# Performance work log

Hardware: AMD Instinct MI355X
Metric: run time of the kernel (lower is better)

The kernel has to match this reference:

```python
import jax, jax.numpy as jnp
import numpy as np

N_NODES = 100000
N_EDGES = 3200000
F_IN = 256
HID = 64
N_CLS = 16


def setup_inputs() -> dict:
    key = jax.random.key(0)
    ks = jax.random.split(key, 12)
    x = jax.random.normal(ks[0], (N_NODES, F_IN), dtype=jnp.float32)
    edge_index = jax.random.randint(ks[1], (2, N_EDGES), 0, N_NODES, dtype=jnp.int32)
    w_mul = jax.random.normal(ks[2], (N_EDGES, 1), dtype=jnp.float32)
    s1 = 1.0 / np.sqrt(F_IN)
    s2 = 1.0 / np.sqrt(HID)
    # layer 1 params
    lin1_w = jax.random.uniform(ks[3], (HID, F_IN), minval=-s1, maxval=s1, dtype=jnp.float32)
    lin1_b = jax.random.uniform(ks[4], (HID,), minval=-s1, maxval=s1, dtype=jnp.float32)
    mlp1_w0 = jax.random.uniform(ks[5], (HID, 1), minval=-1.0, maxval=1.0, dtype=jnp.float32)
    mlp1_w1 = jax.random.uniform(ks[6], (HID, HID), minval=-s2, maxval=s2, dtype=jnp.float32)
    mlp1_b1 = jax.random.uniform(ks[7], (HID,), minval=-s2, maxval=s2, dtype=jnp.float32)
    # layer 2 params
    lin2_w = jax.random.uniform(ks[8], (N_CLS, HID), minval=-s2, maxval=s2, dtype=jnp.float32)
    lin2_b = jax.random.uniform(ks[9], (N_CLS,), minval=-s2, maxval=s2, dtype=jnp.float32)
    mlp2_w0 = jax.random.uniform(ks[10], (HID, 1), minval=-1.0, maxval=1.0, dtype=jnp.float32)
    mlp2_w1 = jax.random.uniform(ks[11], (N_CLS, HID), minval=-s2, maxval=s2, dtype=jnp.float32)
    mlp2_b1 = jnp.zeros((N_CLS,), dtype=jnp.float32)
    return dict(x=x, edge_index=edge_index, w_mul=w_mul,
                lin1_w=lin1_w, lin1_b=lin1_b, mlp1_w0=mlp1_w0, mlp1_w1=mlp1_w1, mlp1_b1=mlp1_b1,
                lin2_w=lin2_w, lin2_b=lin2_b, mlp2_w0=mlp2_w0, mlp2_w1=mlp2_w1, mlp2_b1=mlp2_b1)


def curv_layer(x, src, dst, w_mul, lin_w, lin_b, m_w0, m_w1, m_b1, n_nodes):
    # dense projection: [N, out]
    h = x @ lin_w.T + lin_b
    # per-edge weight MLP: Linear(1,HID,no bias) -> LeakyReLU(0.2) -> Linear(HID,out,bias)
    ew = jax.nn.leaky_relu(w_mul @ m_w0.T, negative_slope=0.2) @ m_w1.T + m_b1  # [E, out]
    # segment softmax keyed by source node (PyG softmax(out_weight, edge_index[0]))
    emax = jax.ops.segment_max(ew, src, num_segments=n_nodes)  # [N, out]
    e = jnp.exp(ew - emax[src])
    esum = jax.ops.segment_sum(e, src, num_segments=n_nodes)
    alpha = e / (esum[src] + 1e-16)  # [E, out]
    # message = alpha * x_j (x_j = h[src]); scatter-add at destination
    msg = alpha * h[src]
    return jax.ops.segment_sum(msg, dst, num_segments=n_nodes)  # [N, out]


def reference(x, edge_index, w_mul,
              lin1_w, lin1_b, mlp1_w0, mlp1_w1, mlp1_b1,
              lin2_w, lin2_b, mlp2_w0, mlp2_w1, mlp2_b1):
    src, dst = edge_index[0], edge_index[1]
    n = x.shape[0]
    # eval mode: dropout(p=0.8) is identity
    h = curv_layer(x, src, dst, w_mul, lin1_w, lin1_b, mlp1_w0, mlp1_w1, mlp1_b1, n)
    h = jax.nn.elu(h)
    h = curv_layer(h, src, dst, w_mul, lin2_w, lin2_b, mlp2_w0, mlp2_w1, mlp2_b1, n)
    return jax.nn.log_softmax(h, axis=1)
```

## Files before the change

kernel.cpp:

```cpp
#include <hip/hip_runtime.h>
#include <math.h>

#define FIN 256
#define HID 64
#define NCLS 16
#define BSH 8
#define BWD (1 << BSH)
#define NBKMAX 512
#define CAP 9216
#define CHUNK_S 8192
#define CHUNK_D 4096

typedef __attribute__((ext_vector_type(8))) short bf16x8;
typedef __attribute__((ext_vector_type(4))) float f32x4;

__global__ __launch_bounds__(512) void init_kernel(int* gcur_s, int* gcur_d) {
    int tid = threadIdx.x;
    gcur_s[tid] = tid * CAP;
    gcur_d[tid] = tid * CAP;
}

__global__ __launch_bounds__(512) void stage_kernel(const int* __restrict__ ei,
                                                    const float* __restrict__ w,
                                                    int* gcur_s, int* gcur_d,
                                                    unsigned int* st_s, uint2* st_d,
                                                    int E, int nchunk_s) {
    __shared__ int lh[NBKMAX];
    __shared__ int lofs[NBKMAX];
    __shared__ int lcur[NBKMAX];
    __shared__ int gbase[NBKMAX];
    __shared__ int wsum[8];
    __shared__ uint2 buf2[CHUNK_D];
    unsigned int* buf1 = (unsigned int*)buf2;
    int tid = threadIdx.x;
    int wv = tid >> 6, lane = tid & 63;
    int side = (blockIdx.x >= nchunk_s) ? 1 : 0;
    lh[tid] = 0;
    __syncthreads();
    if (!side) {
        int base = blockIdx.x * CHUNK_S;
        #pragma unroll
        for (int j = 0; j < CHUNK_S / 512; j++) {
            int e = base + tid + j * 512;
            if (e < E) atomicAdd(&lh[((unsigned)ei[e]) >> BSH], 1);
        }
    } else {
        int base = (blockIdx.x - nchunk_s) * CHUNK_D;
        #pragma unroll
        for (int j = 0; j < CHUNK_D / 512; j++) {
            int e = base + tid + j * 512;
            if (e < E) atomicAdd(&lh[((unsigned)ei[E + e]) >> BSH], 1);
        }
    }
    __syncthreads();
    int v = lh[tid];
    int inc = v;
    #pragma unroll
    for (int off = 1; off < 64; off <<= 1) {
        int p = __shfl_up(inc, off);
        if (lane >= off) inc += p;
    }
    if (lane == 63) wsum[wv] = inc;
    __syncthreads();
    int pre = 0;
    #pragma unroll
    for (int j = 0; j < 8; j++) pre += (j < wv) ? wsum[j] : 0;
    int ex = pre + inc - v;
    lofs[tid] = ex;
    lcur[tid] = ex;
    __syncthreads();
    if (!side) {
        int base = blockIdx.x * CHUNK_S;
        #pragma unroll
        for (int j = 0; j < CHUNK_S / 512; j++) {
            int e = base + tid + j * 512;
            if (e < E) {
                int s = ei[e];
                unsigned int rec = (__float_as_uint(w[e]) & 0xFFFFFF00u) | (unsigned int)(s & 0xFF);
                int p = atomicAdd(&lcur[((unsigned)s) >> BSH], 1);
                buf1[p] = rec;
            }
        }
    } else {
        int base = (blockIdx.x - nchunk_s) * CHUNK_D;
        #pragma unroll
        for (int j = 0; j < CHUNK_D / 512; j++) {
            int e = base + tid + j * 512;
            if (e < E) {
                int d = ei[E + e];
                int s = ei[e];
                unsigned int rec = (__float_as_uint(w[e]) & 0xFFFFFF00u) | (unsigned int)(d & 0xFF);
                int p = atomicAdd(&lcur[((unsigned)d) >> BSH], 1);
                buf2[p] = make_uint2((unsigned int)s, rec);
            }
        }
    }
    __syncthreads();
    {
        int c = lh[tid];
        if (c) gbase[tid] = atomicAdd(side ? &gcur_d[tid] : &gcur_s[tid], c);
    }
    __syncthreads();
    int sub = lane >> 4, ln = lane & 15;
    if (!side) {
        for (int b0 = wv * 64; b0 < wv * 64 + 64; b0 += 4) {
            int b = b0 + sub;
            int c = lh[b];
            int ls = lofs[b], gs = gbase[b];
            for (int i = ln; i < c; i += 16) st_s[gs + i] = buf1[ls + i];
        }
    } else {
        for (int b0 = wv * 64; b0 < wv * 64 + 64; b0 += 4) {
            int b = b0 + sub;
            int c = lh[b];
            int ls = lofs[b], gs = gbase[b];
            for (int i = ln; i < c; i += 16) st_d[gs + i] = buf2[ls + i];
        }
    }
}

__global__ __launch_bounds__(512) void bucket_scan_kernel(const int* gcur_s, const int* gcur_d,
                                                          int* bbase_s, int* bbase_d,
                                                          int* offs_s, int* offs_d,
                                                          int N, int nbk, int E) {
    int side = blockIdx.x;
    const int* gc = side ? gcur_d : gcur_s;
    int* bb = side ? bbase_d : bbase_s;
    __shared__ int tmp[512];
    int tid = threadIdx.x;
    int v = (tid < nbk) ? (gc[tid] - tid * CAP) : 0;
    tmp[tid] = v;
    __syncthreads();
    for (int off = 1; off < 512; off <<= 1) {
        int add = (tid >= off) ? tmp[tid - off] : 0;
        __syncthreads();
        tmp[tid] += add;
        __syncthreads();
    }
    if (tid < nbk) bb[tid] = tmp[tid] - v;
    if (tid == 0) {
        bb[nbk] = E;
        (side ? offs_d : offs_s)[N] = E;
    }
}

__global__ __launch_bounds__(256) void bucket_build_s_kernel(const int* __restrict__ bbase,
                                                             const unsigned int* __restrict__ st,
                                                             int* offs, float* t_s, int N) {
    int b = blockIdx.x;
    int r0 = bbase[b];
    int cnt = bbase[b + 1] - r0;
    if (cnt > CAP) cnt = CAP;
    size_t sb = (size_t)b * CAP;
    int n0 = b << BSH;
    int nn = min(BWD, N - n0);
    __shared__ int lh[BWD];
    __shared__ int lofs[BWD];
    __shared__ float buf[CAP];
    int tid = threadIdx.x;
    lh[tid] = 0;
    __syncthreads();
    for (int i = tid; i < cnt; i += 256) atomicAdd(&lh[st[sb + i] & 0xFFu], 1);
    __syncthreads();
    int v = lh[tid];
    lofs[tid] = v;
    __syncthreads();
    for (int off = 1; off < 256; off <<= 1) {
        int add = (tid >= off) ? lofs[tid - off] : 0;
        __syncthreads();
        lofs[tid] += add;
        __syncthreads();
    }
    int ex = lofs[tid] - v;
    if (tid < nn) offs[n0 + tid] = r0 + ex;
    lofs[tid] = ex;
    __syncthreads();
    for (int i = tid; i < cnt; i += 256) {
        unsigned int rec = st[sb + i];
        int p = atomicAdd(&lofs[rec & 0xFFu], 1);
        buf[p] = __uint_as_float(rec & 0xFFFFFF00u);
    }
    __syncthreads();
    for (int i = tid; i < cnt; i += 256) t_s[r0 + i] = buf[i];
}

__global__ __launch_bounds__(256) void bucket_build_d_kernel(const int* __restrict__ bbase,
                                                             const uint2* __restrict__ st,
                                                             int* offs, int2* ed, int N) {
    int b = blockIdx.x;
    int r0 = bbase[b];
    int cnt = bbase[b + 1] - r0;
    if (cnt > CAP) cnt = CAP;
    size_t sb = (size_t)b * CAP;
    int n0 = b << BSH;
    int nn = min(BWD, N - n0);
    __shared__ int lh[BWD];
    __shared__ int lofs[BWD];
    __shared__ int2 buf[CAP];
    int tid = threadIdx.x;
    lh[tid] = 0;
    __syncthreads();
    for (int i = tid; i < cnt; i += 256) atomicAdd(&lh[st[sb + i].y & 0xFFu], 1);
    __syncthreads();
    int v = lh[tid];
    lofs[tid] = v;
    __syncthreads();
    for (int off = 1; off < 256; off <<= 1) {
        int add = (tid >= off) ? lofs[tid - off] : 0;
        __syncthreads();
        lofs[tid] += add;
        __syncthreads();
    }
    int ex = lofs[tid] - v;
    if (tid < nn) offs[n0 + tid] = r0 + ex;
    lofs[tid] = ex;
    __syncthreads();
    for (int i = tid; i < cnt; i += 256) {
        uint2 rec = st[sb + i];
        int p = atomicAdd(&lofs[rec.y & 0xFFu], 1);
        buf[p] = make_int2((int)rec.x, (int)(rec.y & 0xFFFFFF00u));
    }
    __syncthreads();
    for (int i = tid; i < cnt; i += 256) ed[r0 + i] = buf[i];
}

#define LOG2E 1.44269504088896340736f
__global__ void prep_kernel(const float* __restrict__ w0a, const float* __restrict__ w1a,
                            const float* __restrict__ w0b, const float* __restrict__ w1b,
                            float* Ap1, float* An1, float* Ap2, float* An2) {
    int tid = threadIdx.x;
    if (tid < 64) {
        float ap = 0.f, an = 0.f;
        for (int j = 0; j < 64; j++) {
            float w0 = w0a[j];
            float w1 = w1a[tid * 64 + j];
            ap += w0 * ((w0 >= 0.f) ? 1.f : 0.2f) * w1;
            an += w0 * ((w0 <= 0.f) ? 1.f : 0.2f) * w1;
        }
        Ap1[tid] = ap * LOG2E; An1[tid] = an * LOG2E;
    } else if (tid < 80) {
        int k = tid - 64;
        float ap = 0.f, an = 0.f;
        for (int j = 0; j < 64; j++) {
            float w0 = w0b[j];
            float w1 = w1b[k * 64 + j];
            ap += w0 * ((w0 >= 0.f) ? 1.f : 0.2f) * w1;
            an += w0 * ((w0 <= 0.f) ? 1.f : 0.2f) * w1;
        }
        Ap2[k] = ap * LOG2E; An2[k] = an * LOG2E;
    }
}

__global__ __launch_bounds__(256) void esum_kernel(const int* __restrict__ offs,
                                                   const float* __restrict__ t_s,
                                                   const float* __restrict__ Ap1,
                                                   const float* __restrict__ An1,
                                                   const float* __restrict__ Ap2,
                                                   const float* __restrict__ An2,
                                                   float* __restrict__ inv1,
                                                   float* __restrict__ inv2, int N) {
    int node = blockIdx.x * 4 + (threadIdx.x >> 6);
    int k = threadIdx.x & 63;
    if (node >= N) return;
    int s0 = offs[node], s1 = offs[node + 1];
    float ap = Ap1[k], an = An1[k];
    bool lo = (k < 16);
    float ap2 = lo ? Ap2[k] : 0.f;
    float an2 = lo ? An2[k] : 0.f;
    float sum = 0.f, sum2 = 0.f;
    int i = s0;
    for (; i + 3 < s1; i += 4) {
        float t0 = t_s[i], t1 = t_s[i + 1], t2 = t_s[i + 2], t3 = t_s[i + 3];
        sum += __builtin_amdgcn_exp2f(t0 * ((t0 >= 0.f) ? ap : an));
        sum += __builtin_amdgcn_exp2f(t1 * ((t1 >= 0.f) ? ap : an));
        sum += __builtin_amdgcn_exp2f(t2 * ((t2 >= 0.f) ? ap : an));
        sum += __builtin_amdgcn_exp2f(t3 * ((t3 >= 0.f) ? ap : an));
        if (lo) {
            sum2 += __builtin_amdgcn_exp2f(t0 * ((t0 >= 0.f) ? ap2 : an2));
            sum2 += __builtin_amdgcn_exp2f(t1 * ((t1 >= 0.f) ? ap2 : an2));
            sum2 += __builtin_amdgcn_exp2f(t2 * ((t2 >= 0.f) ? ap2 : an2));
            sum2 += __builtin_amdgcn_exp2f(t3 * ((t3 >= 0.f) ? ap2 : an2));
        }
    }
    for (; i < s1; i++) {
        float t = t_s[i];
        sum += __builtin_amdgcn_exp2f(t * ((t >= 0.f) ? ap : an));
        if (lo) sum2 += __builtin_amdgcn_exp2f(t * ((t >= 0.f) ? ap2 : an2));
    }
    inv1[(size_t)node * 64 + k] = (s1 > s0) ? 1.f / (sum + 1e-16f) : 0.f;
    if (lo) inv2[(size_t)node * 16 + k] = (s1 > s0) ? 1.f / (sum2 + 1e-16f) : 0.f;
}

__device__ __forceinline__ unsigned int bf16rn(float f) {
    unsigned int u = __float_as_uint(f);
    return (u + 0x7fffu + ((u >> 16) & 1u)) >> 16;
}

__device__ __forceinline__ void cvt8_split(const float4 a, const float4 b, bf16x8& h, bf16x8& l) {
    float f[8] = {a.x, a.y, a.z, a.w, b.x, b.y, b.z, b.w};
    #pragma unroll
    for (int j = 0; j < 8; j++) {
        unsigned int uh = bf16rn(f[j]);
        float hf = __uint_as_float(uh << 16);
        float r = f[j] - hf;
        unsigned int ul = bf16rn(r);
        h[j] = (short)uh;
        l[j] = (short)ul;
    }
}

#define KCH 64
__global__ __launch_bounds__(256, 4) void gemm1_kernel(const float* __restrict__ x,
                                                       const float* __restrict__ W,
                                                       const float* __restrict__ b,
                                                       const float* __restrict__ inv,
                                                       uint2* __restrict__ g1, int N) {
    __shared__ unsigned short xh[64 * KCH];
    __shared__ unsigned short xl[64 * KCH];
    __shared__ unsigned short wh[64 * KCH];
    __shared__ unsigned short wl[64 * KCH];
    int tid = threadIdx.x;
    int block_row = blockIdx.x * 64;
    float4 pf[4][2];
    auto load_chunk = [&](int kbase) {
        #pragma unroll
        for (int i = 0; i < 4; i++) {
            int t = tid + i * 256;
            if (t < 512) {
                int r = t >> 3, g = t & 7;
                int gr = block_row + r;
                if (gr < N) {
                    const float* p = &x[(size_t)gr * FIN + kbase + g * 8];
                    pf[i][0] = *(const float4*)p;
                    pf[i][1] = *(const float4*)(p + 4);
                } else {
                    pf[i][0] = make_float4(0.f, 0.f, 0.f, 0.f);
                    pf[i][1] = make_float4(0.f, 0.f, 0.f, 0.f);
                }
            } else {
                int r = (t - 512) >> 3, g = t & 7;
                const float* p = &W[r * FIN + kbase + g * 8];
                pf[i][0] = *(const float4*)p;
                pf[i][1] = *(const float4*)(p + 4);
            }
        }
    };
    auto write_chunk = [&]() {
        #pragma unroll
        for (int i = 0; i < 4; i++) {
            int t = tid + i * 256;
            int r = (t & 511) >> 3, g = t & 7;
            int gs = g ^ (r & 7);
            bf16x8 h, l;
            cvt8_split(pf[i][0], pf[i][1], h, l);
            if (t < 512) {
                *(bf16x8*)&xh[r * KCH + gs * 8] = h;
                *(bf16x8*)&xl[r * KCH + gs * 8] = l;
            } else {
                *(bf16x8*)&wh[r * KCH + gs * 8] = h;
                *(bf16x8*)&wl[r * KCH + gs * 8] = l;
            }
        }
    };

    int wv = tid >> 6, l = tid & 63;
    int lrow = l & 15, kg = l >> 4;
    f32x4 acc[4];
    #pragma unroll
    for (int c = 0; c < 4; c++) acc[c] = (f32x4){0.f, 0.f, 0.f, 0.f};

    const unsigned short* xrow_h = &xh[(wv * 16 + lrow) * KCH];
    const unsigned short* xrow_l = &xl[(wv * 16 + lrow) * KCH];

    load_chunk(0);
    for (int kc = 0; kc < FIN / KCH; kc++) {
        write_chunk();
        __syncthreads();
        if (kc + 1 < FIN / KCH) load_chunk((kc + 1) * KCH);
        #pragma unroll
        for (int s = 0; s < 2; s++) {
            int gB = ((s * 4 + kg) ^ (lrow & 7)) * 8;
            bf16x8 bh = *(const bf16x8*)&xrow_h[gB];
            bf16x8 bl = *(const bf16x8*)&xrow_l[gB];
            #pragma unroll
            for (int c = 0; c < 4; c++) {
                int wro = (c * 16 + lrow) * KCH + gB;
                bf16x8 ah = *(const bf16x8*)&wh[wro];
                bf16x8 al = *(const bf16x8*)&wl[wro];
                acc[c] = __builtin_amdgcn_mfma_f32_16x16x32_bf16(ah, bh, acc[c], 0, 0, 0);
                acc[c] = __builtin_amdgcn_mfma_f32_16x16x32_bf16(ah, bl, acc[c], 0, 0, 0);
                acc[c] = __builtin_amdgcn_mfma_f32_16x16x32_bf16(al, bh, acc[c], 0, 0, 0);
            }
        }
        __syncthreads();
    }
    int node = block_row + wv * 16 + lrow;
    if (node < N) {
        #pragma unroll
        for (int c = 0; c < 4; c++) {
            int colb = c * 16 + kg * 4;
            float4 bv = *(const float4*)&b[colb];
            float4 iv = *(const float4*)&inv[(size_t)node * 64 + colb];
            float o0 = (acc[c].x + bv.x) * iv.x;
            float o1 = (acc[c].y + bv.y) * iv.y;
            float o2 = (acc[c].z + bv.z) * iv.z;
            float o3 = (acc[c].w + bv.w) * iv.w;
            uint2 p;
            p.x = bf16rn(o0) | (bf16rn(o1) << 16);
            p.y = bf16rn(o2) | (bf16rn(o3) << 16);
            g1[(size_t)node * 16 + (colb >> 2)] = p;
        }
    }
}

#define GP 68
__global__ __launch_bounds__(256) void gemm2_kernel(const float* __restrict__ x2,
                                                    const float* __restrict__ W2,
                                                    const float* __restrict__ b2,
                                                    const float* __restrict__ inv,
                                                    float* __restrict__ g2, int N) {
    __shared__ float ws[16][GP];
    __shared__ float xs[16][GP];
    __shared__ float bs[16];
    int tid = threadIdx.x;
    {
        int c = tid >> 4, j4 = tid & 15;
        float4 v = ((const float4*)W2)[tid];
        ws[c][j4 * 4 + 0] = v.x; ws[c][j4 * 4 + 1] = v.y;
        ws[c][j4 * 4 + 2] = v.z; ws[c][j4 * 4 + 3] = v.w;
    }
    if (tid < 16) bs[tid] = b2[tid];
    int node0 = blockIdx.x * 16;
    {
        int r = tid >> 4, c4 = tid & 15;
        int gn = node0 + r;
        float4 v = (gn < N) ? *(const float4*)&x2[(size_t)gn * 64 + c4 * 4]
                            : make_float4(0.f, 0.f, 0.f, 0.f);
        xs[r][c4 * 4 + 0] = v.x; xs[r][c4 * 4 + 1] = v.y;
        xs[r][c4 * 4 + 2] = v.z; xs[r][c4 * 4 + 3] = v.w;
    }
    __syncthreads();
    int node_l = tid >> 4, col = tid & 15;
    int gn = node0 + node_l;
    if (gn >= N) return;
    float acc = bs[col];
    #pragma unroll
    for (int j4 = 0; j4 < 16; j4++) {
        float4 xv = *(const float4*)&xs[node_l][j4 * 4];
        float4 wv = *(const float4*)&ws[col][j4 * 4];
        acc += xv.x * wv.x + xv.y * wv.y + xv.z * wv.z + xv.w * wv.w;
    }
    g2[(size_t)gn * NCLS + col] = acc * inv[(size_t)gn * NCLS + col];
}

__global__ __launch_bounds__(256) void agg1_kernel(const int* __restrict__ offs,
                                                   const int2* __restrict__ ed,
                                                   const float* __restrict__ Ap,
                                                   const float* __restrict__ An,
                                                   const uint4* __restrict__ g,
                                                   float* __restrict__ x2, int N) {
    int node = blockIdx.x * 32 + (threadIdx.x >> 3);
    int l = threadIdx.x & 7;
    if (node >= N) return;
    int d0 = offs[node], d1 = offs[node + 1];
    float4 ap0 = ((const float4*)Ap)[l * 2], ap1 = ((const float4*)Ap)[l * 2 + 1];
    float4 an0 = ((const float4*)An)[l * 2], an1 = ((const float4*)An)[l * 2 + 1];
    float4 acc0 = make_float4(0.f, 0.f, 0.f, 0.f);
    float4 acc1 = make_float4(0.f, 0.f, 0.f, 0.f);
    int i = d0;
    int end4 = d0 + ((d1 - d0) & ~3);
    for (; i < end4; i += 4) {
        int2 e[4];
        #pragma unroll
        for (int j = 0; j < 4; j++) e[j] = ed[i + j];
        uint4 gv[4];
        #pragma unroll
        for (int j = 0; j < 4; j++)
            gv[j] = g[((size_t)e[j].x << 3) + l];
        #pragma unroll
        for (int j = 0; j < 4; j++) {
            float t = __int_as_float(e[j].y);
            float4 a0 = (t >= 0.f) ? ap0 : an0;
            float4 a1 = (t >= 0.f) ? ap1 : an1;
            acc0.x += __builtin_amdgcn_exp2f(t * a0.x) * __uint_as_float(gv[j].x << 16);
            acc0.y += __builtin_amdgcn_exp2f(t * a0.y) * __uint_as_float(gv[j].x & 0xffff0000u);
            acc0.z += __builtin_amdgcn_exp2f(t * a0.z) * __uint_as_float(gv[j].y << 16);
            acc0.w += __builtin_amdgcn_exp2f(t * a0.w) * __uint_as_float(gv[j].y & 0xffff0000u);
            acc1.x += __builtin_amdgcn_exp2f(t * a1.x) * __uint_as_float(gv[j].z << 16);
            acc1.y += __builtin_amdgcn_exp2f(t * a1.y) * __uint_as_float(gv[j].z & 0xffff0000u);
            acc1.z += __builtin_amdgcn_exp2f(t * a1.z) * __uint_as_float(gv[j].w << 16);
            acc1.w += __builtin_amdgcn_exp2f(t * a1.w) * __uint_as_float(gv[j].w & 0xffff0000u);
        }
    }
    for (; i < d1; i++) {
        int2 e = ed[i];
        float t = __int_as_float(e.y);
        float4 a0 = (t >= 0.f) ? ap0 : an0;
        float4 a1 = (t >= 0.f) ? ap1 : an1;
        uint4 gv = g[((size_t)e.x << 3) + l];
        acc0.x += __builtin_amdgcn_exp2f(t * a0.x) * __uint_as_float(gv.x << 16);
        acc0.y += __builtin_amdgcn_exp2f(t * a0.y) * __uint_as_float(gv.x & 0xffff0000u);
        acc0.z += __builtin_amdgcn_exp2f(t * a0.z) * __uint_as_float(gv.y << 16);
        acc0.w += __builtin_amdgcn_exp2f(t * a0.w) * __uint_as_float(gv.y & 0xffff0000u);
        acc1.x += __builtin_amdgcn_exp2f(t * a1.x) * __uint_as_float(gv.z << 16);
        acc1.y += __builtin_amdgcn_exp2f(t * a1.y) * __uint_as_float(gv.z & 0xffff0000u);
        acc1.z += __builtin_amdgcn_exp2f(t * a1.z) * __uint_as_float(gv.w << 16);
        acc1.w += __builtin_amdgcn_exp2f(t * a1.w) * __uint_as_float(gv.w & 0xffff0000u);
    }
    float4 o0, o1;
    o0.x = (acc0.x > 0.f) ? acc0.x : (__expf(acc0.x) - 1.f);
    o0.y = (acc0.y > 0.f) ? acc0.y : (__expf(acc0.y) - 1.f);
    o0.z = (acc0.z > 0.f) ? acc0.z : (__expf(acc0.z) - 1.f);
    o0.w = (acc0.w > 0.f) ? acc0.w : (__expf(acc0.w) - 1.f);
    o1.x = (acc1.x > 0.f) ? acc1.x : (__expf(acc1.x) - 1.f);
    o1.y = (acc1.y > 0.f) ? acc1.y : (__expf(acc1.y) - 1.f);
    o1.z = (acc1.z > 0.f) ? acc1.z : (__expf(acc1.z) - 1.f);
    o1.w = (acc1.w > 0.f) ? acc1.w : (__expf(acc1.w) - 1.f);
    float* dst = x2 + ((size_t)node << 6) + l * 8;
    *(float4*)(dst) = o0;
    *(float4*)(dst + 4) = o1;
}

__global__ __launch_bounds__(256) void agg2_kernel(const int* __restrict__ offs,
                                                   const int2* __restrict__ ed,
                                                   const float* __restrict__ Ap,
                                                   const float* __restrict__ An,
                                                   const float* __restrict__ g,
                                                   float* __restrict__ out, int N) {
    int node = blockIdx.x * 64 + (threadIdx.x >> 2);
    int l = threadIdx.x & 3;
    if (node >= N) return;
    int d0 = offs[node], d1 = offs[node + 1];
    float4 ap = ((const float4*)Ap)[l];
    float4 an = ((const float4*)An)[l];
    float4 acc = make_float4(0.f, 0.f, 0.f, 0.f);
    int i = d0;
    int end8 = d0 + ((d1 - d0) & ~7);
    for (; i < end8; i += 8) {
        int2 e[8];
        #pragma unroll
        for (int j = 0; j < 8; j++) e[j] = ed[i + j];
        float4 gv[8];
        #pragma unroll
        for (int j = 0; j < 8; j++)
            gv[j] = *(const float4*)(g + ((size_t)e[j].x << 4) + l * 4);
        #pragma unroll
        for (int j = 0; j < 8; j++) {
            float t = __int_as_float(e[j].y);
            float4 a = (t >= 0.f) ? ap : an;
            acc.x += __builtin_amdgcn_exp2f(t * a.x) * gv[j].x;
            acc.y += __builtin_amdgcn_exp2f(t * a.y) * gv[j].y;
            acc.z += __builtin_amdgcn_exp2f(t * a.z) * gv[j].z;
            acc.w += __builtin_amdgcn_exp2f(t * a.w) * gv[j].w;
        }
    }
    for (; i < d1; i++) {
        int2 e = ed[i];
        float t = __int_as_float(e.y);
        float4 a = (t >= 0.f) ? ap : an;
        float4 gv = *(const float4*)(g + ((size_t)e.x << 4) + l * 4);
        acc.x += __builtin_amdgcn_exp2f(t * a.x) * gv.x;
        acc.y += __builtin_amdgcn_exp2f(t * a.y) * gv.y;
        acc.z += __builtin_amdgcn_exp2f(t * a.z) * gv.z;
        acc.w += __builtin_amdgcn_exp2f(t * a.w) * gv.w;
    }
    float m = fmaxf(fmaxf(acc.x, acc.y), fmaxf(acc.z, acc.w));
    m = fmaxf(m, __shfl_xor(m, 1, 4));
    m = fmaxf(m, __shfl_xor(m, 2, 4));
    float s = __expf(acc.x - m) + __expf(acc.y - m) + __expf(acc.z - m) + __expf(acc.w - m);
    s += __shfl_xor(s, 1, 4);
    s += __shfl_xor(s, 2, 4);
    float lse = m + __logf(s);
    float4 o = make_float4(acc.x - lse, acc.y - lse, acc.z - lse, acc.w - lse);
    *(float4*)(out + ((size_t)node << 4) + l * 4) = o;
}

extern "C" void kernel_launch(void* const* d_in, const int* in_sizes, int n_in,
                              void* d_out, int out_size, void* d_ws, size_t ws_size,
                              hipStream_t stream) {
    const float* x      = (const float*)d_in[0];
    const int*   ei     = (const int*)d_in[1];
    const float* wmul   = (const float*)d_in[2];
    const float* lin1_w = (const float*)d_in[3];
    const float* lin1_b = (const float*)d_in[4];
    const float* m1w0   = (const float*)d_in[5];
    const float* m1w1   = (const float*)d_in[6];
    const float* lin2_w = (const float*)d_in[8];
    const float* lin2_b = (const float*)d_in[9];
    const float* m2w0   = (const float*)d_in[10];
    const float* m2w1   = (const float*)d_in[11];

    int N = in_sizes[0] / FIN;
    int E = in_sizes[1] / 2;
    int nbk = (N + BWD - 1) >> BSH;
    int nchunk_s = (E + CHUNK_S - 1) / CHUNK_S;
    int nchunk_d = (E + CHUNK_D - 1) / CHUNK_D;

    char* ws = (char*)d_ws;
    auto alloc = [&](size_t bytes) {
        char* p = ws;
        ws += (bytes + 255) & ~(size_t)255;
        return p;
    };
    int*   gcur_s  = (int*)alloc(NBKMAX * 4);
    int*   gcur_d  = (int*)alloc(NBKMAX * 4);
    int*   bbase_s = (int*)alloc((NBKMAX + 1) * 4);
    int*   bbase_d = (int*)alloc((NBKMAX + 1) * 4);
    float* Ap1     = (float*)alloc(64 * 4);
    float* An1     = (float*)alloc(64 * 4);
    float* Ap2     = (float*)alloc(16 * 4);
    float* An2     = (float*)alloc(16 * 4);
    int*   offs_s  = (int*)alloc((size_t)(N + 1) * 4);
    int*   offs_d  = (int*)alloc((size_t)(N + 1) * 4);
    float* t_s     = (float*)alloc((size_t)E * 4);
    int2*  ed      = (int2*)alloc((size_t)E * 8);
    char*  reg = ws;
    unsigned int* st_s = (unsigned int*)(reg);
    uint2*        st_d = (uint2*)(reg + (((size_t)nbk * CAP * 4 + 255) & ~(size_t)255));
    float* inv1 = (float*)(reg);
    float* x2   = (float*)(reg);
    char*  regB = reg + (((size_t)N * 64 * 4 + 255) & ~(size_t)255);
    uint2* g1   = (uint2*)(regB);
    float* inv2 = (float*)(regB + ((size_t)N * 16 * 8));
    float* g2   = (float*)(regB + ((size_t)N * 16 * 8) + ((size_t)N * 16 * 4));

    init_kernel<<<1, 512, 0, stream>>>(gcur_s, gcur_d);
    prep_kernel<<<1, 128, 0, stream>>>(m1w0, m1w1, m2w0, m2w1, Ap1, An1, Ap2, An2);
    stage_kernel<<<nchunk_s + nchunk_d, 512, 0, stream>>>(ei, wmul, gcur_s, gcur_d,
                                                          st_s, st_d, E, nchunk_s);
    bucket_scan_kernel<<<2, 512, 0, stream>>>(gcur_s, gcur_d, bbase_s, bbase_d,
                                              offs_s, offs_d, N, nbk, E);
    bucket_build_s_kernel<<<nbk, 256, 0, stream>>>(bbase_s, st_s, offs_s, t_s, N);
    bucket_build_d_kernel<<<nbk, 256, 0, stream>>>(bbase_d, st_d, offs_d, ed, N);
    esum_kernel<<<(N + 3) / 4, 256, 0, stream>>>(offs_s, t_s, Ap1, An1, Ap2, An2, inv1, inv2, N);
    gemm1_kernel<<<(N + 63) / 64, 256, 0, stream>>>(x, lin1_w, lin1_b, inv1, g1, N);
    agg1_kernel<<<(N + 31) / 32, 256, 0, stream>>>(offs_d, ed, Ap1, An1, (const uint4*)g1, x2, N);
    gemm2_kernel<<<(N + 15) / 16, 256, 0, stream>>>(x2, lin2_w, lin2_b, inv2, g2, N);
    agg2_kernel<<<(N + 63) / 64, 256, 0, stream>>>(offs_d, ed, Ap2, An2, g2, (float*)d_out, N);
}
```

Measured before the change: 485.1 us.

## Partition source segments by weight sign and split esum into per-layer kernels

Bucket build now sorts each source node's edges by the sign bit of the edge weight and records a midpoint offset. The exp-sum loop can then use a fixed positive or negative slope per subsegment, with no per-edge select. The combined esum kernel is split into a 64-wide layer-1 kernel and a 16-wide layer-2 kernel, so 48 of 64 lanes no longer sit idle on the layer-2 sum. This costs an extra launch, a second pass over t_s, a mid array, and a larger histogram in shared memory.

```diff
diff --git a/kernel.cpp b/kernel.cpp
--- a/kernel.cpp
+++ b/kernel.cpp
@@ -146,7 +146,7 @@
 
 __global__ __launch_bounds__(256) void bucket_build_s_kernel(const int* __restrict__ bbase,
                                                              const unsigned int* __restrict__ st,
-                                                             int* offs, float* t_s, int N) {
+                                                             int* offs, int* mid, float* t_s, int N) {
     int b = blockIdx.x;
     int r0 = bbase[b];
     int cnt = bbase[b + 1] - r0;
@@ -154,30 +154,40 @@
     size_t sb = (size_t)b * CAP;
     int n0 = b << BSH;
     int nn = min(BWD, N - n0);
-    __shared__ int lh[BWD];
-    __shared__ int lofs[BWD];
+    __shared__ int lh[2 * BWD];
+    __shared__ int lscan[BWD];
+    __shared__ int lcur[2 * BWD];
     __shared__ float buf[CAP];
     int tid = threadIdx.x;
     lh[tid] = 0;
-    __syncthreads();
-    for (int i = tid; i < cnt; i += 256) atomicAdd(&lh[st[sb + i] & 0xFFu], 1);
-    __syncthreads();
-    int v = lh[tid];
-    lofs[tid] = v;
-    __syncthreads();
-    for (int off = 1; off < 256; off <<= 1) {
-        int add = (tid >= off) ? lofs[tid - off] : 0;
-        __syncthreads();
-        lofs[tid] += add;
-        __syncthreads();
-    }
-    int ex = lofs[tid] - v;
-    if (tid < nn) offs[n0 + tid] = r0 + ex;
-    lofs[tid] = ex;
+    lh[tid + BWD] = 0;
     __syncthreads();
     for (int i = tid; i < cnt; i += 256) {
         unsigned int rec = st[sb + i];
-        int p = atomicAdd(&lofs[rec & 0xFFu], 1);
+        atomicAdd(&lh[((rec & 0xFFu) << 1) | (rec >> 31)], 1);
+    }
+    __syncthreads();
+    int c0 = lh[2 * tid], c1 = lh[2 * tid + 1];
+    int v = c0 + c1;
+    lscan[tid] = v;
+    __syncthreads();
+    for (int off = 1; off < 256; off <<= 1) {
+        int add = (tid >= off) ? lscan[tid - off] : 0;
+        __syncthreads();
+        lscan[tid] += add;
+        __syncthreads();
+    }
+    int ex = lscan[tid] - v;
+    if (tid < nn) {
+        offs[n0 + tid] = r0 + ex;
+        mid[n0 + tid] = r0 + ex + c0;
+    }
+    lcur[2 * tid] = ex;
+    lcur[2 * tid + 1] = ex + c0;
+    __syncthreads();
+    for (int i = tid; i < cnt; i += 256) {
+        unsigned int rec = st[sb + i];
+        int p = atomicAdd(&lcur[((rec & 0xFFu) << 1) | (rec >> 31)], 1);
         buf[p] = __uint_as_float(rec & 0xFFFFFF00u);
     }
     __syncthreads();
@@ -251,44 +261,46 @@
     }
 }
 
-__global__ __launch_bounds__(256) void esum_kernel(const int* __restrict__ offs,
-                                                   const float* __restrict__ t_s,
-                                                   const float* __restrict__ Ap1,
-                                                   const float* __restrict__ An1,
-                                                   const float* __restrict__ Ap2,
-                                                   const float* __restrict__ An2,
-                                                   float* __restrict__ inv1,
-                                                   float* __restrict__ inv2, int N) {
+__device__ __forceinline__ float seg_expsum(const float* __restrict__ t, int i0, int i1, float a) {
+    float sum = 0.f;
+    int i = i0;
+    for (; i + 3 < i1; i += 4) {
+        float t0 = t[i], t1 = t[i + 1], t2 = t[i + 2], t3 = t[i + 3];
+        sum += __builtin_amdgcn_exp2f(t0 * a);
+        sum += __builtin_amdgcn_exp2f(t1 * a);
+        sum += __builtin_amdgcn_exp2f(t2 * a);
+        sum += __builtin_amdgcn_exp2f(t3 * a);
+    }
+    for (; i < i1; i++) sum += __builtin_amdgcn_exp2f(t[i] * a);
+    return sum;
+}
+
+__global__ __launch_bounds__(256) void esum1_kernel(const int* __restrict__ offs,
+                                                    const int* __restrict__ mid,
+                                                    const float* __restrict__ t_s,
+                                                    const float* __restrict__ Ap,
+                                                    const float* __restrict__ An,
+                                                    float* __restrict__ inv, int N) {
     int node = blockIdx.x * 4 + (threadIdx.x >> 6);
     int k = threadIdx.x & 63;
     if (node >= N) return;
-    int s0 = offs[node], s1 = offs[node + 1];
-    float ap = Ap1[k], an = An1[k];
-    bool lo = (k < 16);
-    float ap2 = lo ? Ap2[k] : 0.f;
-    float an2 = lo ? An2[k] : 0.f;
-    float sum = 0.f, sum2 = 0.f;
-    int i = s0;
-    for (; i + 3 < s1; i += 4) {
-        float t0 = t_s[i], t1 = t_s[i + 1], t2 = t_s[i + 2], t3 = t_s[i + 3];
-        sum += __builtin_amdgcn_exp2f(t0 * ((t0 >= 0.f) ? ap : an));
-        sum += __builtin_amdgcn_exp2f(t1 * ((t1 >= 0.f) ? ap : an));
-        sum += __builtin_amdgcn_exp2f(t2 * ((t2 >= 0.f) ? ap : an));
-        sum += __builtin_amdgcn_exp2f(t3 * ((t3 >= 0.f) ? ap : an));
-        if (lo) {
-            sum2 += __builtin_amdgcn_exp2f(t0 * ((t0 >= 0.f) ? ap2 : an2));
-            sum2 += __builtin_amdgcn_exp2f(t1 * ((t1 >= 0.f) ? ap2 : an2));
-            sum2 += __builtin_amdgcn_exp2f(t2 * ((t2 >= 0.f) ? ap2 : an2));
-            sum2 += __builtin_amdgcn_exp2f(t3 * ((t3 >= 0.f) ? ap2 : an2));
-        }
-    }
-    for (; i < s1; i++) {
-        float t = t_s[i];
-        sum += __builtin_amdgcn_exp2f(t * ((t >= 0.f) ? ap : an));
-        if (lo) sum2 += __builtin_amdgcn_exp2f(t * ((t >= 0.f) ? ap2 : an2));
-    }
-    inv1[(size_t)node * 64 + k] = (s1 > s0) ? 1.f / (sum + 1e-16f) : 0.f;
-    if (lo) inv2[(size_t)node * 16 + k] = (s1 > s0) ? 1.f / (sum2 + 1e-16f) : 0.f;
+    int s0 = offs[node], m = mid[node], s1 = offs[node + 1];
+    float sum = seg_expsum(t_s, s0, m, Ap[k]) + seg_expsum(t_s, m, s1, An[k]);
+    inv[(size_t)node * 64 + k] = (s1 > s0) ? 1.f / (sum + 1e-16f) : 0.f;
+}
+
+__global__ __launch_bounds__(256) void esum2_kernel(const int* __restrict__ offs,
+                                                    const int* __restrict__ mid,
+                                                    const float* __restrict__ t_s,
+                                                    const float* __restrict__ Ap,
+                                                    const float* __restrict__ An,
+                                                    float* __restrict__ inv, int N) {
+    int node = blockIdx.x * 16 + (threadIdx.x >> 4);
+    int k = threadIdx.x & 15;
+    if (node >= N) return;
+    int s0 = offs[node], m = mid[node], s1 = offs[node + 1];
+    float sum = seg_expsum(t_s, s0, m, Ap[k]) + seg_expsum(t_s, m, s1, An[k]);
+    inv[(size_t)node * 16 + k] = (s1 > s0) ? 1.f / (sum + 1e-16f) : 0.f;
 }
 
 __device__ __forceinline__ unsigned int bf16rn(float f) {
@@ -612,6 +624,7 @@
     float* An2     = (float*)alloc(16 * 4);
     int*   offs_s  = (int*)alloc((size_t)(N + 1) * 4);
     int*   offs_d  = (int*)alloc((size_t)(N + 1) * 4);
+    int*   mid_s   = (int*)alloc((size_t)N * 4);
     float* t_s     = (float*)alloc((size_t)E * 4);
     int2*  ed      = (int2*)alloc((size_t)E * 8);
     char*  reg = ws;
@@ -630,11 +643,12 @@
                                                           st_s, st_d, E, nchunk_s);
     bucket_scan_kernel<<<2, 512, 0, stream>>>(gcur_s, gcur_d, bbase_s, bbase_d,
                                               offs_s, offs_d, N, nbk, E);
-    bucket_build_s_kernel<<<nbk, 256, 0, stream>>>(bbase_s, st_s, offs_s, t_s, N);
+    bucket_build_s_kernel<<<nbk, 256, 0, stream>>>(bbase_s, st_s, offs_s, mid_s, t_s, N);
     bucket_build_d_kernel<<<nbk, 256, 0, stream>>>(bbase_d, st_d, offs_d, ed, N);
-    esum_kernel<<<(N + 3) / 4, 256, 0, stream>>>(offs_s, t_s, Ap1, An1, Ap2, An2, inv1, inv2, N);
+    esum1_kernel<<<(N + 3) / 4, 256, 0, stream>>>(offs_s, mid_s, t_s, Ap1, An1, inv1, N);
     gemm1_kernel<<<(N + 63) / 64, 256, 0, stream>>>(x, lin1_w, lin1_b, inv1, g1, N);
     agg1_kernel<<<(N + 31) / 32, 256, 0, stream>>>(offs_d, ed, Ap1, An1, (const uint4*)g1, x2, N);
+    esum2_kernel<<<(N + 15) / 16, 256, 0, stream>>>(offs_s, mid_s, t_s, Ap2, An2, inv2, N);
     gemm2_kernel<<<(N + 15) / 16, 256, 0, stream>>>(x2, lin2_w, lin2_b, inv2, g2, N);
     agg2_kernel<<<(N + 63) / 64, 256, 0, stream>>>(offs_d, ed, Ap2, An2, g2, (float*)d_out, N);
 }
```

Result: no change. 487.9 us (+0.6%).
